# Kernel optimization log

Measured on AMD Instinct MI355X. Metric: run time of the kernel, lower is better.

The kernel has to match this reference:

```python
import jax, jax.numpy as jnp
import numpy as np

NUM_HEADS = 4


def setup_inputs() -> dict:
    key = jax.random.key(0)
    k1, k2, k3 = jax.random.split(key, 3)
    B, NN, C = 1, 256, 128
    x = jax.random.normal(k1, (B, NN, C), dtype=jnp.float32)
    # Linear(d_model, 4*d_model, bias=False); stored as (in, out) for x @ W_w
    W_w = jax.random.normal(k2, (C, 4 * C), dtype=jnp.float32) * (C ** -0.5)
    # proj = Linear(d_model, d_model) with bias; stored as (in, out)
    W_proj = jax.random.normal(k3, (C, C), dtype=jnp.float32) * (C ** -0.5)
    b_proj = jnp.zeros((C,), dtype=jnp.float32)
    return {"x": x, "W_w": W_w, "W_proj": W_proj, "b_proj": b_proj}


def reference(x, W_w, W_proj, b_proj):
    B, NN, C = x.shape
    H = NUM_HEADS
    D = C // H
    scale = D ** -0.5
    # qkv-style projection: (B, NN, 4, H, D) -> (4, B, H, NN, D)
    w = (x @ W_w).reshape(B, NN, 4, H, D).transpose(2, 0, 3, 1, 4)
    a, b, c, v = w[0], w[1], w[2], w[3]
    AB = jnp.einsum('bhid,bhjd->bhij', a, b) * scale
    CD = jnp.einsum('bhid,bhkd->bhik', a, c) * scale
    EF = jnp.einsum('bhjd,bhkd->bhjk', b, c) * scale
    # Triplet scores: (B, H, NN, NN, NN)
    A_ijk = AB[..., :, :, None] + CD[..., :, None, :] + EF[..., None, :, :]
    e = jnp.exp(A_ijk)
    # Normalize over (i, j) for each k, per original sum(dim=(-2,-3))
    norm = jnp.clip(e.sum(axis=(-2, -3), keepdims=True), 1e-6, None)
    en = e / norm
    x1 = jnp.einsum('bhijk,bhjd->bhid', en, v)
    x2 = jnp.einsum('bhijk,bhkd->bhid', en, v)
    out = (x1 * x2).transpose(0, 2, 1, 3).reshape(B, NN, C)
    return out @ W_proj + b_proj
```

## Files before the change

kernel.cpp:

```cpp
#include <hip/hip_runtime.h>
#include <hip/hip_bf16.h>


constexpr size_t OFF_W     = 0;
constexpr size_t OFF_P     = 131072;
constexpr size_t OFF_Q     = OFF_P + 262144;
constexpr size_t OFF_RT    = OFF_Q + 262144;
constexpr size_t OFF_T     = OFF_RT + 262144;
constexpr size_t OFF_S     = OFF_T + 524288;
constexpr size_t OFF_NORMP = OFF_S + 524288;

__global__ __launch_bounds__(256) void k_w(const float* __restrict__ x,
                                           const float* __restrict__ Ww,
                                           float* __restrict__ w,
                                           const float* __restrict__ bp,
                                           float* __restrict__ out) {
    __shared__ __align__(16) float As[1152];
    __shared__ __align__(16) float Bs[1152];
    int j0 = blockIdx.x * 32, i0 = blockIdx.y * 32;
    int t = threadIdx.x, tx = t & 15, ty = t >> 4, r = t >> 3, g = t & 7;
    {
        int oidx = (blockIdx.y * 16 + blockIdx.x) * 256 + t;
        out[oidx] = bp[oidx & 127];
    }
    float4 a4 = *(const float4*)&x[(size_t)(i0 + r) * 128 + g * 4];
    float4 b4 = *(const float4*)&Ww[(size_t)r * 512 + j0 + g * 4];
    float a00 = 0, a01 = 0, a10 = 0, a11 = 0;
    for (int kc = 0; kc < 128; kc += 32) {
        As[(g * 4 + 0) * 36 + r] = a4.x; As[(g * 4 + 1) * 36 + r] = a4.y;
        As[(g * 4 + 2) * 36 + r] = a4.z; As[(g * 4 + 3) * 36 + r] = a4.w;
        *(float4*)&Bs[r * 36 + g * 4] = b4;
        __syncthreads();
        if (kc + 32 < 128) {
            a4 = *(const float4*)&x[(size_t)(i0 + r) * 128 + kc + 32 + g * 4];
            b4 = *(const float4*)&Ww[(size_t)(kc + 32 + r) * 512 + j0 + g * 4];
        }
#pragma unroll
        for (int kk = 0; kk < 32; kk++) {
            float2 av = *(float2*)&As[kk * 36 + ty * 2];
            float2 bv = *(float2*)&Bs[kk * 36 + tx * 2];
            a00 += av.x * bv.x; a01 += av.x * bv.y;
            a10 += av.y * bv.x; a11 += av.y * bv.y;
        }
        __syncthreads();
    }
    *(float2*)&w[(size_t)(i0 + ty * 2) * 512 + j0 + tx * 2] = make_float2(a00, a01);
    *(float2*)&w[(size_t)(i0 + ty * 2 + 1) * 512 + j0 + tx * 2] = make_float2(a10, a11);
}

__global__ __launch_bounds__(256, 2) void k_T(const float* __restrict__ w,
                                              float* __restrict__ P,
                                              float* __restrict__ Q,
                                              float* __restrict__ Rt,
                                              float* __restrict__ T,
                                              float* __restrict__ normp) {
    __shared__ __align__(16) float aT[1152];
    __shared__ __align__(16) float cT[1152];
    __shared__ __align__(16) float bT[1152];
    __shared__ __align__(16) float Ps[1152];
    __shared__ __align__(16) float Rs[1152];
    int h = blockIdx.z >> 1, jh = blockIdx.z & 1;
    int k0 = blockIdx.x * 32, i0 = blockIdx.y * 32;
    int jc0 = jh * 128;
    size_t hb = (size_t)h * 65536;
    int t = threadIdx.x, tx = t & 15, ty = t >> 4, r = t >> 3, g = t & 7;
    const float sc = 0.17677669529663687f;

    float4 av = *(const float4*)&w[(size_t)(i0 + r) * 512 + h * 32 + g * 4];
    aT[(g * 4 + 0) * 36 + r] = av.x; aT[(g * 4 + 1) * 36 + r] = av.y;
    aT[(g * 4 + 2) * 36 + r] = av.z; aT[(g * 4 + 3) * 36 + r] = av.w;
    float4 cv = *(const float4*)&w[(size_t)(k0 + r) * 512 + 256 + h * 32 + g * 4];
    cT[(g * 4 + 0) * 36 + r] = cv.x; cT[(g * 4 + 1) * 36 + r] = cv.y;
    cT[(g * 4 + 2) * 36 + r] = cv.z; cT[(g * 4 + 3) * 36 + r] = cv.w;
    float4 bv = *(const float4*)&w[(size_t)(jc0 + r) * 512 + 128 + h * 32 + g * 4];
    __syncthreads();

    float dq00 = 0, dq01 = 0, dq10 = 0, dq11 = 0;
#pragma unroll
    for (int d = 0; d < 32; d++) {
        float2 a2 = *(float2*)&aT[d * 36 + ty * 2];
        float2 c2 = *(float2*)&cT[d * 36 + tx * 2];
        dq00 += a2.x * c2.x; dq01 += a2.x * c2.y;
        dq10 += a2.y * c2.x; dq11 += a2.y * c2.y;
    }
    float q00 = __expf(sc * dq00), q01 = __expf(sc * dq01);
    float q10 = __expf(sc * dq10), q11 = __expf(sc * dq11);
    if (jh == 0) {
        *(float2*)&Q[hb + (size_t)(i0 + ty * 2) * 256 + k0 + tx * 2] = make_float2(q00, q01);
        *(float2*)&Q[hb + (size_t)(i0 + ty * 2 + 1) * 256 + k0 + tx * 2] = make_float2(q10, q11);
    }

    const bool wP = (k0 == 0), wR = (blockIdx.y == 0);
    float acc00 = 0, acc01 = 0, acc10 = 0, acc11 = 0;
    for (int jc = jc0; jc < jc0 + 128; jc += 32) {
        bT[(g * 4 + 0) * 36 + r] = bv.x; bT[(g * 4 + 1) * 36 + r] = bv.y;
        bT[(g * 4 + 2) * 36 + r] = bv.z; bT[(g * 4 + 3) * 36 + r] = bv.w;
        __syncthreads();
        if (jc + 32 < jc0 + 128)
            bv = *(const float4*)&w[(size_t)(jc + 32 + r) * 512 + 128 + h * 32 + g * 4];
        float dp00 = 0, dp01 = 0, dp10 = 0, dp11 = 0;
        float dr00 = 0, dr01 = 0, dr10 = 0, dr11 = 0;
#pragma unroll
        for (int d = 0; d < 32; d++) {
            float2 b2 = *(float2*)&bT[d * 36 + ty * 2];
            float2 a2 = *(float2*)&aT[d * 36 + tx * 2];
            float2 c2 = *(float2*)&cT[d * 36 + tx * 2];
            dp00 += b2.x * a2.x; dp01 += b2.x * a2.y;
            dp10 += b2.y * a2.x; dp11 += b2.y * a2.y;
            dr00 += b2.x * c2.x; dr01 += b2.x * c2.y;
            dr10 += b2.y * c2.x; dr11 += b2.y * c2.y;
        }
        float p00 = __expf(sc * dp00), p01 = __expf(sc * dp01);
        float p10 = __expf(sc * dp10), p11 = __expf(sc * dp11);
        float r00 = __expf(sc * dr00), r01 = __expf(sc * dr01);
        float r10 = __expf(sc * dr10), r11 = __expf(sc * dr11);
        *(float2*)&Ps[(ty * 2 + 0) * 36 + tx * 2] = make_float2(p00, p01);
        *(float2*)&Ps[(ty * 2 + 1) * 36 + tx * 2] = make_float2(p10, p11);
        *(float2*)&Rs[(ty * 2 + 0) * 36 + tx * 2] = make_float2(r00, r01);
        *(float2*)&Rs[(ty * 2 + 1) * 36 + tx * 2] = make_float2(r10, r11);
        if (wP) {
            *(float2*)&P[hb + (size_t)(i0 + tx * 2 + 0) * 256 + jc + ty * 2] = make_float2(p00, p10);
            *(float2*)&P[hb + (size_t)(i0 + tx * 2 + 1) * 256 + jc + ty * 2] = make_float2(p01, p11);
        }
        if (wR) {
            *(float2*)&Rt[hb + (size_t)(k0 + tx * 2 + 0) * 256 + jc + ty * 2] = make_float2(r00, r10);
            *(float2*)&Rt[hb + (size_t)(k0 + tx * 2 + 1) * 256 + jc + ty * 2] = make_float2(r01, r11);
        }
        __syncthreads();
#pragma unroll
        for (int j = 0; j < 32; j++) {
            float2 p2 = *(float2*)&Ps[j * 36 + ty * 2];
            float2 r2 = *(float2*)&Rs[j * 36 + tx * 2];
            acc00 += p2.x * r2.x; acc01 += p2.x * r2.y;
            acc10 += p2.y * r2.x; acc11 += p2.y * r2.y;
        }
    }
    float* Tp = T + (size_t)jh * 262144;
    *(float2*)&Tp[hb + (size_t)(i0 + ty * 2) * 256 + k0 + tx * 2] = make_float2(acc00, acc01);
    *(float2*)&Tp[hb + (size_t)(i0 + ty * 2 + 1) * 256 + k0 + tx * 2] = make_float2(acc10, acc11);
    __syncthreads();
    float* red = Ps;
    red[ty * 34 + tx * 2]     = q00 * acc00 + q10 * acc10;
    red[ty * 34 + tx * 2 + 1] = q01 * acc01 + q11 * acc11;
    __syncthreads();
    if (t < 32) {
        float s = 0.f;
#pragma unroll
        for (int m = 0; m < 16; m++) s += red[m * 34 + t];
        normp[h * 4096 + (jh * 8 + blockIdx.y) * 256 + k0 + t] = s;
    }
}

__global__ __launch_bounds__(256, 2) void k_S(const float* __restrict__ Q,
                                              const float* __restrict__ Rt,
                                              const float* __restrict__ normp,
                                              float* __restrict__ S) {
    __shared__ __align__(16) float As[1152];
    __shared__ __align__(16) float Bs[1152];
    __shared__ float rn_s[256];
    int h = blockIdx.z >> 1, kh = blockIdx.z & 1;
    int j0 = blockIdx.x * 32, i0 = blockIdx.y * 32;
    int kc0 = kh * 128;
    size_t hb = (size_t)h * 65536;
    int t = threadIdx.x, tx = t & 15, ty = t >> 4, r = t >> 3, g = t & 7;
    {
        float s = 0.f;
#pragma unroll
        for (int ib = 0; ib < 16; ib++) s += normp[h * 4096 + ib * 256 + t];
        rn_s[t] = 1.f / fmaxf(s, 1e-6f);
    }
    float4 a4 = *(const float4*)&Q[hb + (size_t)(i0 + r) * 256 + kc0 + g * 4];
    float4 b4 = *(const float4*)&Rt[hb + (size_t)(kc0 + r) * 256 + j0 + g * 4];
    __syncthreads();
    float a00 = 0, a01 = 0, a10 = 0, a11 = 0;
    for (int kc = kc0; kc < kc0 + 128; kc += 32) {
        As[(g * 4 + 0) * 36 + r] = a4.x * rn_s[kc + g * 4 + 0];
        As[(g * 4 + 1) * 36 + r] = a4.y * rn_s[kc + g * 4 + 1];
        As[(g * 4 + 2) * 36 + r] = a4.z * rn_s[kc + g * 4 + 2];
        As[(g * 4 + 3) * 36 + r] = a4.w * rn_s[kc + g * 4 + 3];
        *(float4*)&Bs[r * 36 + g * 4] = b4;
        __syncthreads();
        if (kc + 32 < kc0 + 128) {
            a4 = *(const float4*)&Q[hb + (size_t)(i0 + r) * 256 + kc + 32 + g * 4];
            b4 = *(const float4*)&Rt[hb + (size_t)(kc + 32 + r) * 256 + j0 + g * 4];
        }
#pragma unroll
        for (int kk = 0; kk < 32; kk++) {
            float2 av = *(float2*)&As[kk * 36 + ty * 2];
            float2 bv = *(float2*)&Bs[kk * 36 + tx * 2];
            a00 += av.x * bv.x; a01 += av.x * bv.y;
            a10 += av.y * bv.x; a11 += av.y * bv.y;
        }
        __syncthreads();
    }
    float* Sp = S + (size_t)kh * 262144;
    *(float2*)&Sp[hb + (size_t)(i0 + ty * 2) * 256 + j0 + tx * 2] = make_float2(a00, a01);
    *(float2*)&Sp[hb + (size_t)(i0 + ty * 2 + 1) * 256 + j0 + tx * 2] = make_float2(a10, a11);
}

__global__ __launch_bounds__(256) void k_x1x2(
    const float* __restrict__ P, const float* __restrict__ Q,
    const float* __restrict__ S, const float* __restrict__ T,
    const float* __restrict__ normp, const float* __restrict__ w,
    const float* __restrict__ Wp, float* __restrict__ out) {
    int h = blockIdx.y;
    int i0 = blockIdx.x * 8;
    size_t hb = (size_t)h * 65536;
    __shared__ __align__(16) float wp[2048];
    __shared__ __align__(16) float wq[2048];
    __shared__ __align__(16) float vls[8192];
    __shared__ float rn_s[256];
    int t = threadIdx.x;
    {
        float s = 0.f;
#pragma unroll
        for (int ib = 0; ib < 16; ib++) s += normp[h * 4096 + ib * 256 + t];
        rn_s[t] = 1.f / fmaxf(s, 1e-6f);
    }
    __syncthreads();
#pragma unroll
    for (int m = 0; m < 2; m++) {
        int lin = (m * 256 + t) * 4;
        int rr = lin >> 8, jj = lin & 255;
        size_t o = hb + (size_t)(i0 + rr) * 256 + jj;
        float4 p4 = *(const float4*)&P[o];
        float4 s4a = *(const float4*)&S[o];
        float4 s4b = *(const float4*)&S[o + 262144];
        float4 q4 = *(const float4*)&Q[o];
        float4 t4a = *(const float4*)&T[o];
        float4 t4b = *(const float4*)&T[o + 262144];
        float4 wpv, wqv;
        wpv.x = p4.x * (s4a.x + s4b.x); wpv.y = p4.y * (s4a.y + s4b.y);
        wpv.z = p4.z * (s4a.z + s4b.z); wpv.w = p4.w * (s4a.w + s4b.w);
        wqv.x = q4.x * (t4a.x + t4b.x) * rn_s[jj + 0];
        wqv.y = q4.y * (t4a.y + t4b.y) * rn_s[jj + 1];
        wqv.z = q4.z * (t4a.z + t4b.z) * rn_s[jj + 2];
        wqv.w = q4.w * (t4a.w + t4b.w) * rn_s[jj + 3];
        *(float4*)&wp[rr * 256 + jj] = wpv;
        *(float4*)&wq[rr * 256 + jj] = wqv;
    }
#pragma unroll
    for (int m = 0; m < 8; m++) {
        int lin = (m * 256 + t) * 4;
        int jj = lin >> 5, dd = lin & 31;
        *(float4*)&vls[jj * 32 + dd] =
            *(const float4*)&w[(size_t)jj * 512 + 384 + h * 32 + dd];
    }
    __syncthreads();
    int d = t & 31, rl = t >> 5;
    float x1 = 0.f, x2 = 0.f;
#pragma unroll 8
    for (int j = 0; j < 256; j++) {
        float vv = vls[j * 32 + d];
        x1 += wp[rl * 256 + j] * vv;
        x2 += wq[rl * 256 + j] * vv;
    }
    float yv = x1 * x2;
    __syncthreads();
    float* ys = wp;
    float* Wps = vls;
    ys[rl * 33 + d] = yv;
#pragma unroll
    for (int m = 0; m < 4; m++) {
        int idx = m * 256 + t;
        int lin = idx * 4;
        int k = lin >> 7, n = lin & 127;
        *(float4*)&Wps[k * 128 + n] =
            *(const float4*)&Wp[(size_t)(h * 32 + k) * 128 + n];
    }
    __syncthreads();
    int n = t & 127, ti = t >> 7;
    float acc0 = 0, acc1 = 0, acc2 = 0, acc3 = 0;
#pragma unroll
    for (int k = 0; k < 32; k++) {
        float wv = Wps[k * 128 + n];
        acc0 += ys[(ti + 0) * 33 + k] * wv;
        acc1 += ys[(ti + 2) * 33 + k] * wv;
        acc2 += ys[(ti + 4) * 33 + k] * wv;
        acc3 += ys[(ti + 6) * 33 + k] * wv;
    }
    atomicAdd(&out[(size_t)(i0 + ti + 0) * 128 + n], acc0);
    atomicAdd(&out[(size_t)(i0 + ti + 2) * 128 + n], acc1);
    atomicAdd(&out[(size_t)(i0 + ti + 4) * 128 + n], acc2);
    atomicAdd(&out[(size_t)(i0 + ti + 6) * 128 + n], acc3);
}

extern "C" void kernel_launch(void* const* d_in, const int* in_sizes, int n_in,
                              void* d_out, int out_size, void* d_ws, size_t ws_size,
                              hipStream_t stream) {
    const float* x      = (const float*)d_in[0];
    const float* W_w    = (const float*)d_in[1];
    const float* W_proj = (const float*)d_in[2];
    const float* b_proj = (const float*)d_in[3];
    float* out = (float*)d_out;
    float* ws  = (float*)d_ws;

    float* w     = ws + OFF_W;
    float* P     = ws + OFF_P;
    float* Q     = ws + OFF_Q;
    float* Rt    = ws + OFF_RT;
    float* T     = ws + OFF_T;
    float* S     = ws + OFF_S;
    float* normp = ws + OFF_NORMP;

    k_w<<<dim3(16, 8), 256, 0, stream>>>(x, W_w, w, b_proj, out);
    k_T<<<dim3(8, 8, 8), 256, 0, stream>>>(w, P, Q, Rt, T, normp);
    k_S<<<dim3(8, 8, 8), 256, 0, stream>>>(Q, Rt, normp, S);
    k_x1x2<<<dim3(32, 4), 256, 0, stream>>>(P, Q, S, T, normp, w, W_proj, out);
}
```

Baseline: 41.57 us.

## Transpose shared tiles for float4 inner-product loads and split x1x2 work finer

In k_T and k_S the shared-memory tiles are stored transposed so each inner loop reads float4 vectors along the reduction dimension, cutting LDS instruction count. k_T also caches the a and c columns in registers across the j-chunk loop. k_x1x2 processes 4 rows per block instead of 8, doubling the grid, stores V transposed, and splits the j reduction across two thread halves with a shared-memory combine. This raises register pressure (64 float2 held in registers) and changes floating-point summation order, which could lower occupancy.

New measurement: 39.77 us. -4.3%, faster.

```diff
diff --git a/kernel.cpp b/kernel.cpp
--- a/kernel.cpp
+++ b/kernel.cpp
@@ -57,8 +57,8 @@
     __shared__ __align__(16) float aT[1152];
     __shared__ __align__(16) float cT[1152];
     __shared__ __align__(16) float bT[1152];
-    __shared__ __align__(16) float Ps[1152];
-    __shared__ __align__(16) float Rs[1152];
+    __shared__ __align__(16) float PsT[1152];
+    __shared__ __align__(16) float RsT[1152];
     int h = blockIdx.z >> 1, jh = blockIdx.z & 1;
     int k0 = blockIdx.x * 32, i0 = blockIdx.y * 32;
     int jc0 = jh * 128;
@@ -75,11 +75,18 @@
     float4 bv = *(const float4*)&w[(size_t)(jc0 + r) * 512 + 128 + h * 32 + g * 4];
     __syncthreads();
 
+    float2 a_tx[32], c_tx[32];
+#pragma unroll
+    for (int d = 0; d < 32; d++) {
+        a_tx[d] = *(float2*)&aT[d * 36 + 2 * tx];
+        c_tx[d] = *(float2*)&cT[d * 36 + 2 * tx];
+    }
+
     float dq00 = 0, dq01 = 0, dq10 = 0, dq11 = 0;
 #pragma unroll
     for (int d = 0; d < 32; d++) {
-        float2 a2 = *(float2*)&aT[d * 36 + ty * 2];
-        float2 c2 = *(float2*)&cT[d * 36 + tx * 2];
+        float2 a2 = *(float2*)&aT[d * 36 + 2 * ty];
+        float2 c2 = c_tx[d];
         dq00 += a2.x * c2.x; dq01 += a2.x * c2.y;
         dq10 += a2.y * c2.x; dq11 += a2.y * c2.y;
     }
@@ -102,9 +109,9 @@
         float dr00 = 0, dr01 = 0, dr10 = 0, dr11 = 0;
 #pragma unroll
         for (int d = 0; d < 32; d++) {
-            float2 b2 = *(float2*)&bT[d * 36 + ty * 2];
-            float2 a2 = *(float2*)&aT[d * 36 + tx * 2];
-            float2 c2 = *(float2*)&cT[d * 36 + tx * 2];
+            float2 b2 = *(float2*)&bT[d * 36 + 2 * ty];
+            float2 a2 = a_tx[d];
+            float2 c2 = c_tx[d];
             dp00 += b2.x * a2.x; dp01 += b2.x * a2.y;
             dp10 += b2.y * a2.x; dp11 += b2.y * a2.y;
             dr00 += b2.x * c2.x; dr01 += b2.x * c2.y;
@@ -114,10 +121,10 @@
         float p10 = __expf(sc * dp10), p11 = __expf(sc * dp11);
         float r00 = __expf(sc * dr00), r01 = __expf(sc * dr01);
         float r10 = __expf(sc * dr10), r11 = __expf(sc * dr11);
-        *(float2*)&Ps[(ty * 2 + 0) * 36 + tx * 2] = make_float2(p00, p01);
-        *(float2*)&Ps[(ty * 2 + 1) * 36 + tx * 2] = make_float2(p10, p11);
-        *(float2*)&Rs[(ty * 2 + 0) * 36 + tx * 2] = make_float2(r00, r01);
-        *(float2*)&Rs[(ty * 2 + 1) * 36 + tx * 2] = make_float2(r10, r11);
+        *(float2*)&PsT[(2 * tx + 0) * 36 + 2 * ty] = make_float2(p00, p10);
+        *(float2*)&PsT[(2 * tx + 1) * 36 + 2 * ty] = make_float2(p01, p11);
+        *(float2*)&RsT[(2 * tx + 0) * 36 + 2 * ty] = make_float2(r00, r10);
+        *(float2*)&RsT[(2 * tx + 1) * 36 + 2 * ty] = make_float2(r01, r11);
         if (wP) {
             *(float2*)&P[hb + (size_t)(i0 + tx * 2 + 0) * 256 + jc + ty * 2] = make_float2(p00, p10);
             *(float2*)&P[hb + (size_t)(i0 + tx * 2 + 1) * 256 + jc + ty * 2] = make_float2(p01, p11);
@@ -128,18 +135,22 @@
         }
         __syncthreads();
 #pragma unroll
-        for (int j = 0; j < 32; j++) {
-            float2 p2 = *(float2*)&Ps[j * 36 + ty * 2];
-            float2 r2 = *(float2*)&Rs[j * 36 + tx * 2];
-            acc00 += p2.x * r2.x; acc01 += p2.x * r2.y;
-            acc10 += p2.y * r2.x; acc11 += p2.y * r2.y;
+        for (int q = 0; q < 8; q++) {
+            float4 pA = *(float4*)&PsT[(2 * ty + 0) * 36 + 4 * q];
+            float4 pB = *(float4*)&PsT[(2 * ty + 1) * 36 + 4 * q];
+            float4 rA = *(float4*)&RsT[(2 * tx + 0) * 36 + 4 * q];
+            float4 rB = *(float4*)&RsT[(2 * tx + 1) * 36 + 4 * q];
+            acc00 += pA.x * rA.x + pA.y * rA.y + pA.z * rA.z + pA.w * rA.w;
+            acc01 += pA.x * rB.x + pA.y * rB.y + pA.z * rB.z + pA.w * rB.w;
+            acc10 += pB.x * rA.x + pB.y * rA.y + pB.z * rA.z + pB.w * rA.w;
+            acc11 += pB.x * rB.x + pB.y * rB.y + pB.z * rB.z + pB.w * rB.w;
         }
     }
     float* Tp = T + (size_t)jh * 262144;
     *(float2*)&Tp[hb + (size_t)(i0 + ty * 2) * 256 + k0 + tx * 2] = make_float2(acc00, acc01);
     *(float2*)&Tp[hb + (size_t)(i0 + ty * 2 + 1) * 256 + k0 + tx * 2] = make_float2(acc10, acc11);
     __syncthreads();
-    float* red = Ps;
+    float* red = PsT;
     red[ty * 34 + tx * 2]     = q00 * acc00 + q10 * acc10;
     red[ty * 34 + tx * 2 + 1] = q01 * acc01 + q11 * acc11;
     __syncthreads();
@@ -155,8 +166,8 @@
                                               const float* __restrict__ Rt,
                                               const float* __restrict__ normp,
                                               float* __restrict__ S) {
-    __shared__ __align__(16) float As[1152];
-    __shared__ __align__(16) float Bs[1152];
+    __shared__ __align__(16) float AsT[1152];
+    __shared__ __align__(16) float BsT[1152];
     __shared__ float rn_s[256];
     int h = blockIdx.z >> 1, kh = blockIdx.z & 1;
     int j0 = blockIdx.x * 32, i0 = blockIdx.y * 32;
@@ -174,22 +185,30 @@
     __syncthreads();
     float a00 = 0, a01 = 0, a10 = 0, a11 = 0;
     for (int kc = kc0; kc < kc0 + 128; kc += 32) {
-        As[(g * 4 + 0) * 36 + r] = a4.x * rn_s[kc + g * 4 + 0];
-        As[(g * 4 + 1) * 36 + r] = a4.y * rn_s[kc + g * 4 + 1];
-        As[(g * 4 + 2) * 36 + r] = a4.z * rn_s[kc + g * 4 + 2];
-        As[(g * 4 + 3) * 36 + r] = a4.w * rn_s[kc + g * 4 + 3];
-        *(float4*)&Bs[r * 36 + g * 4] = b4;
+        float4 rn4 = *(float4*)&rn_s[kc + g * 4];
+        float4 as4;
+        as4.x = a4.x * rn4.x; as4.y = a4.y * rn4.y;
+        as4.z = a4.z * rn4.z; as4.w = a4.w * rn4.w;
+        *(float4*)&AsT[r * 36 + g * 4] = as4;
+        BsT[(g * 4 + 0) * 36 + r] = b4.x;
+        BsT[(g * 4 + 1) * 36 + r] = b4.y;
+        BsT[(g * 4 + 2) * 36 + r] = b4.z;
+        BsT[(g * 4 + 3) * 36 + r] = b4.w;
         __syncthreads();
         if (kc + 32 < kc0 + 128) {
             a4 = *(const float4*)&Q[hb + (size_t)(i0 + r) * 256 + kc + 32 + g * 4];
             b4 = *(const float4*)&Rt[hb + (size_t)(kc + 32 + r) * 256 + j0 + g * 4];
         }
 #pragma unroll
-        for (int kk = 0; kk < 32; kk++) {
-            float2 av = *(float2*)&As[kk * 36 + ty * 2];
-            float2 bv = *(float2*)&Bs[kk * 36 + tx * 2];
-            a00 += av.x * bv.x; a01 += av.x * bv.y;
-            a10 += av.y * bv.x; a11 += av.y * bv.y;
+        for (int q = 0; q < 8; q++) {
+            float4 aA = *(float4*)&AsT[(2 * ty + 0) * 36 + 4 * q];
+            float4 aB = *(float4*)&AsT[(2 * ty + 1) * 36 + 4 * q];
+            float4 bA = *(float4*)&BsT[(2 * tx + 0) * 36 + 4 * q];
+            float4 bB = *(float4*)&BsT[(2 * tx + 1) * 36 + 4 * q];
+            a00 += aA.x * bA.x + aA.y * bA.y + aA.z * bA.z + aA.w * bA.w;
+            a01 += aA.x * bB.x + aA.y * bB.y + aA.z * bB.z + aA.w * bB.w;
+            a10 += aB.x * bA.x + aB.y * bA.y + aB.z * bA.z + aB.w * bA.w;
+            a11 += aB.x * bB.x + aB.y * bB.y + aB.z * bB.z + aB.w * bB.w;
         }
         __syncthreads();
     }
@@ -204,12 +223,13 @@
     const float* __restrict__ normp, const float* __restrict__ w,
     const float* __restrict__ Wp, float* __restrict__ out) {
     int h = blockIdx.y;
-    int i0 = blockIdx.x * 8;
+    int i0 = blockIdx.x * 4;
     size_t hb = (size_t)h * 65536;
-    __shared__ __align__(16) float wp[2048];
-    __shared__ __align__(16) float wq[2048];
-    __shared__ __align__(16) float vls[8192];
+    __shared__ __align__(16) float wp[1024];
+    __shared__ __align__(16) float wq[1024];
+    __shared__ __align__(16) float vT[8320];
     __shared__ float rn_s[256];
+    __shared__ float ys[144];
     int t = threadIdx.x;
     {
         float s = 0.f;
@@ -218,71 +238,78 @@
         rn_s[t] = 1.f / fmaxf(s, 1e-6f);
     }
     __syncthreads();
-#pragma unroll
-    for (int m = 0; m < 2; m++) {
-        int lin = (m * 256 + t) * 4;
-        int rr = lin >> 8, jj = lin & 255;
+    {
+        int rr = t >> 6, jj = (t & 63) * 4;
         size_t o = hb + (size_t)(i0 + rr) * 256 + jj;
-        float4 p4 = *(const float4*)&P[o];
+        float4 p4  = *(const float4*)&P[o];
         float4 s4a = *(const float4*)&S[o];
         float4 s4b = *(const float4*)&S[o + 262144];
-        float4 q4 = *(const float4*)&Q[o];
+        float4 q4  = *(const float4*)&Q[o];
         float4 t4a = *(const float4*)&T[o];
         float4 t4b = *(const float4*)&T[o + 262144];
+        float4 rn4 = *(float4*)&rn_s[jj];
         float4 wpv, wqv;
         wpv.x = p4.x * (s4a.x + s4b.x); wpv.y = p4.y * (s4a.y + s4b.y);
         wpv.z = p4.z * (s4a.z + s4b.z); wpv.w = p4.w * (s4a.w + s4b.w);
-        wqv.x = q4.x * (t4a.x + t4b.x) * rn_s[jj + 0];
-        wqv.y = q4.y * (t4a.y + t4b.y) * rn_s[jj + 1];
-        wqv.z = q4.z * (t4a.z + t4b.z) * rn_s[jj + 2];
-        wqv.w = q4.w * (t4a.w + t4b.w) * rn_s[jj + 3];
+        wqv.x = q4.x * (t4a.x + t4b.x) * rn4.x;
+        wqv.y = q4.y * (t4a.y + t4b.y) * rn4.y;
+        wqv.z = q4.z * (t4a.z + t4b.z) * rn4.z;
+        wqv.w = q4.w * (t4a.w + t4b.w) * rn4.w;
         *(float4*)&wp[rr * 256 + jj] = wpv;
         *(float4*)&wq[rr * 256 + jj] = wqv;
     }
 #pragma unroll
     for (int m = 0; m < 8; m++) {
-        int lin = (m * 256 + t) * 4;
-        int jj = lin >> 5, dd = lin & 31;
-        *(float4*)&vls[jj * 32 + dd] =
-            *(const float4*)&w[(size_t)jj * 512 + 384 + h * 32 + dd];
-    }
-    __syncthreads();
-    int d = t & 31, rl = t >> 5;
+        int jj = m * 32 + (t >> 3);
+        int dd = (t & 7) * 4;
+        float4 v4 = *(const float4*)&w[(size_t)jj * 512 + 384 + h * 32 + dd];
+        vT[(dd + 0) * 260 + jj] = v4.x;
+        vT[(dd + 1) * 260 + jj] = v4.y;
+        vT[(dd + 2) * 260 + jj] = v4.z;
+        vT[(dd + 3) * 260 + jj] = v4.w;
+    }
+    __syncthreads();
+    int d = t & 31, rl = (t >> 5) & 3, jh2 = t >> 7;
+    int jbase = jh2 * 128;
     float x1 = 0.f, x2 = 0.f;
-#pragma unroll 8
-    for (int j = 0; j < 256; j++) {
-        float vv = vls[j * 32 + d];
-        x1 += wp[rl * 256 + j] * vv;
-        x2 += wq[rl * 256 + j] * vv;
-    }
-    float yv = x1 * x2;
-    __syncthreads();
-    float* ys = wp;
-    float* Wps = vls;
-    ys[rl * 33 + d] = yv;
+#pragma unroll
+    for (int q = 0; q < 32; q++) {
+        int j = jbase + 4 * q;
+        float4 wp4 = *(float4*)&wp[rl * 256 + j];
+        float4 wq4 = *(float4*)&wq[rl * 256 + j];
+        float4 v4  = *(float4*)&vT[d * 260 + j];
+        x1 += wp4.x * v4.x + wp4.y * v4.y + wp4.z * v4.z + wp4.w * v4.w;
+        x2 += wq4.x * v4.x + wq4.y * v4.y + wq4.z * v4.z + wq4.w * v4.w;
+    }
+    __syncthreads();
+    float* redx = wp;
+    float* redy = wq;
+    redx[t] = x1;
+    redy[t] = x2;
+    float* Wps = vT;
 #pragma unroll
     for (int m = 0; m < 4; m++) {
         int idx = m * 256 + t;
-        int lin = idx * 4;
-        int k = lin >> 7, n = lin & 127;
-        *(float4*)&Wps[k * 128 + n] =
-            *(const float4*)&Wp[(size_t)(h * 32 + k) * 128 + n];
+        int k = idx >> 5, n = (idx & 31) * 4;
+        *(float4*)&Wps[k * 128 + n] = *(const float4*)&Wp[(size_t)(h * 32 + k) * 128 + n];
+    }
+    __syncthreads();
+    if (t < 128) {
+        float x1t = redx[t] + redx[t + 128];
+        float x2t = redy[t] + redy[t + 128];
+        ys[rl * 33 + d] = x1t * x2t;
     }
     __syncthreads();
     int n = t & 127, ti = t >> 7;
-    float acc0 = 0, acc1 = 0, acc2 = 0, acc3 = 0;
+    float acc0 = 0.f, acc1 = 0.f;
 #pragma unroll
     for (int k = 0; k < 32; k++) {
         float wv = Wps[k * 128 + n];
         acc0 += ys[(ti + 0) * 33 + k] * wv;
         acc1 += ys[(ti + 2) * 33 + k] * wv;
-        acc2 += ys[(ti + 4) * 33 + k] * wv;
-        acc3 += ys[(ti + 6) * 33 + k] * wv;
     }
     atomicAdd(&out[(size_t)(i0 + ti + 0) * 128 + n], acc0);
     atomicAdd(&out[(size_t)(i0 + ti + 2) * 128 + n], acc1);
-    atomicAdd(&out[(size_t)(i0 + ti + 4) * 128 + n], acc2);
-    atomicAdd(&out[(size_t)(i0 + ti + 6) * 128 + n], acc3);
 }
 
 extern "C" void kernel_launch(void* const* d_in, const int* in_sizes, int n_in,
@@ -306,5 +333,5 @@
     k_w<<<dim3(16, 8), 256, 0, stream>>>(x, W_w, w, b_proj, out);
     k_T<<<dim3(8, 8, 8), 256, 0, stream>>>(w, P, Q, Rt, T, normp);
     k_S<<<dim3(8, 8, 8), 256, 0, stream>>>(Q, Rt, normp, S);
-    k_x1x2<<<dim3(32, 4), 256, 0, stream>>>(P, Q, S, T, normp, w, W_proj, out);
-}
+    k_x1x2<<<dim3(64, 4), 256, 0, stream>>>(P, Q, S, T, normp, w, W_proj, out);
+}
```
